# Kernel optimization log

Hardware: AMD Instinct MI355X
Metric: run time of the kernel (lower is better)

## Reference

```python
import jax, jax.numpy as jnp
import numpy as np

N_HEAD = 16
D_MODEL = 1024
D_HEAD = D_MODEL // N_HEAD  # 64
B, S = 1, 4096


def setup_inputs() -> dict:
    key = jax.random.key(0)
    ks = jax.random.split(key, 7)
    q = jax.random.normal(ks[0], (B, S, D_MODEL), dtype=jnp.float32)
    k = jax.random.normal(ks[1], (B, S, D_MODEL), dtype=jnp.float32)
    v = jax.random.normal(ks[2], (B, S, D_MODEL), dtype=jnp.float32)
    mask = jnp.ones((S, S), dtype=bool)
    # params match torch.rand init (uniform [0,1)); use uniform here too
    w_q = jax.random.uniform(ks[3], (D_MODEL, D_MODEL), dtype=jnp.float32)
    w_k = jax.random.uniform(ks[4], (D_HEAD, D_MODEL), dtype=jnp.float32)
    w_v = jax.random.uniform(ks[5], (D_HEAD, D_MODEL), dtype=jnp.float32)
    w_out = jax.random.uniform(ks[6], (D_MODEL, D_MODEL), dtype=jnp.float32)
    return {"q": q, "k": k, "v": v, "mask": mask,
            "w_q": w_q, "w_k": w_k, "w_v": w_v, "w_out": w_out}


def reference(q, k, v, mask, w_q, w_k, w_v, w_out):
    # F.linear(x, W) == x @ W.T
    query = q @ w_q.T                      # [b, n, d_model]
    key = k @ w_k.T                        # [b, s, d_head]  (single shared KV head)
    value = v @ w_v.T                      # [b, s, d_head]
    b, n, _ = query.shape
    query = query.reshape(b, n, N_HEAD, D_HEAD).transpose(0, 2, 1, 3)  # b h n d
    scores = jnp.einsum('bhnd,bsd->bhns', query, key) / jnp.sqrt(jnp.float32(D_HEAD))
    scores = jnp.where(mask[None, None], scores, jnp.float32(-jnp.inf))
    attn = jax.nn.softmax(scores, axis=-1)             # [b, h, n, s]
    out = jnp.einsum('bhns,bsd->bhnd', attn, value)    # [b, h, n, d]
    out = out.transpose(0, 2, 1, 3).reshape(b, n, D_MODEL)
    return out @ w_out.T
```

## Files before the change

### kernel.cpp

```cpp
#include <hip/hip_runtime.h>
#include <cstdint>
#include <cstddef>

#define S_LEN   4096
#define DM      1024
#define NHEAD   16
#define DH      64

typedef short bf16x8 __attribute__((ext_vector_type(8)));
typedef _Float16 f16x8 __attribute__((ext_vector_type(8)));
typedef float f32x4  __attribute__((ext_vector_type(4)));

__device__ __forceinline__ unsigned short f2bf(float x) {
    uint32_t u = __float_as_uint(x);
    u += 0x7fffu + ((u >> 16) & 1u);
    return (unsigned short)(u >> 16);
}
__device__ __forceinline__ float bf2f(unsigned short u) {
    return __uint_as_float(((uint32_t)u) << 16);
}
__device__ __forceinline__ unsigned pack_bf2(float a, float b) {
    return (unsigned)f2bf(a) | ((unsigned)f2bf(b) << 16);
}
__device__ __forceinline__ unsigned short f2h(float x) {
    _Float16 h = (_Float16)x;
    return __builtin_bit_cast(unsigned short, h);
}
__device__ __forceinline__ unsigned pack_h2(float a, float b) {
    return __builtin_bit_cast(unsigned, __builtin_amdgcn_cvt_pkrtz(a, b));
}
__device__ __forceinline__ void gl_lds16(const unsigned short* g, unsigned short* l) {
    __builtin_amdgcn_global_load_lds(
        (const __attribute__((address_space(1))) unsigned int*)g,
        (__attribute__((address_space(3))) unsigned int*)l, 16, 0, 0);
}
__device__ __forceinline__ void split8(const float4& a0, const float4& a1,
                                       ushort4& h0, ushort4& h1,
                                       ushort4& l0, ushort4& l1) {
    h0.x = f2bf(a0.x); l0.x = f2bf(a0.x - bf2f(h0.x));
    h0.y = f2bf(a0.y); l0.y = f2bf(a0.y - bf2f(h0.y));
    h0.z = f2bf(a0.z); l0.z = f2bf(a0.z - bf2f(h0.z));
    h0.w = f2bf(a0.w); l0.w = f2bf(a0.w - bf2f(h0.w));
    h1.x = f2bf(a1.x); l1.x = f2bf(a1.x - bf2f(h1.x));
    h1.y = f2bf(a1.y); l1.y = f2bf(a1.y - bf2f(h1.y));
    h1.z = f2bf(a1.z); l1.z = f2bf(a1.z - bf2f(h1.z));
    h1.w = f2bf(a1.w); l1.w = f2bf(a1.w - bf2f(h1.w));
}

__global__ void cvt_qw(const float* __restrict__ q, const float* __restrict__ wq,
                       const float* __restrict__ wo,
                       unsigned short* __restrict__ qh, unsigned short* __restrict__ ql,
                       unsigned short* __restrict__ wqh, unsigned short* __restrict__ wql,
                       unsigned short* __restrict__ woh)
{
    const int G1 = 1048576, GW = 262144;
    int i = blockIdx.x * blockDim.x + threadIdx.x;
    const float* src; unsigned short* h; unsigned short* l = nullptr; int off;
    if (i < G1)            { src = q;  h = qh;  l = ql;  off = i; }
    else if (i < G1 + GW)  { src = wq; h = wqh; l = wql; off = i - G1; }
    else                   { src = wo; h = woh;          off = i - G1 - GW; }
    float4 vv = reinterpret_cast<const float4*>(src)[off];
    ushort4 hh;
    hh.x = f2bf(vv.x); hh.y = f2bf(vv.y); hh.z = f2bf(vv.z); hh.w = f2bf(vv.w);
    reinterpret_cast<ushort4*>(h)[off] = hh;
    if (l) {
        ushort4 ll;
        ll.x = f2bf(vv.x - bf2f(hh.x)); ll.y = f2bf(vv.y - bf2f(hh.y));
        ll.z = f2bf(vv.z - bf2f(hh.z)); ll.w = f2bf(vv.w - bf2f(hh.w));
        reinterpret_cast<ushort4*>(l)[off] = ll;
    }
}

__launch_bounds__(256)
__global__ void kv_proj(const float* __restrict__ kin, const float* __restrict__ vin,
                        const float* __restrict__ wk, const float* __restrict__ wv,
                        unsigned short* __restrict__ Kf, unsigned short* __restrict__ Vtf)
{
    __shared__ unsigned short As_h[64][72];
    __shared__ unsigned short Bs_h[64][72];
    __shared__ unsigned short As_l[64][72];
    __shared__ unsigned short Bs_l[64][72];

    const int tid  = threadIdx.x;
    const int wave = tid >> 6;
    const int lane = tid & 63;
    const int lm   = lane & 15;
    const int quad = lane >> 4;
    const int m0   = blockIdx.x * 64;
    const bool isK = (blockIdx.y == 0);
    const float* A = isK ? kin : vin;
    const float* B = isK ? wk : wv;

    f32x4 acc[4] = {};

    for (int kc = 0; kc < DM; kc += 64) {
        __syncthreads();
#pragma unroll
        for (int i = 0; i < 2; ++i) {
            int c   = tid + i * 256;
            int r   = c >> 3;
            int col = (c & 7) * 8;
            float4 a0 = *(const float4*)&A[(size_t)(m0 + r) * DM + kc + col];
            float4 a1 = *(const float4*)&A[(size_t)(m0 + r) * DM + kc + col + 4];
            float4 b0 = *(const float4*)&B[(size_t)r * DM + kc + col];
            float4 b1 = *(const float4*)&B[(size_t)r * DM + kc + col + 4];
            ushort4 h0, h1, l0, l1;
            split8(a0, a1, h0, h1, l0, l1);
            *(ushort4*)&As_h[r][col] = h0;  *(ushort4*)&As_h[r][col + 4] = h1;
            if (isK) { *(ushort4*)&As_l[r][col] = l0;  *(ushort4*)&As_l[r][col + 4] = l1; }
            split8(b0, b1, h0, h1, l0, l1);
            *(ushort4*)&Bs_h[r][col] = h0;  *(ushort4*)&Bs_h[r][col + 4] = h1;
            if (isK) { *(ushort4*)&Bs_l[r][col] = l0;  *(ushort4*)&Bs_l[r][col + 4] = l1; }
        }
        __syncthreads();
#pragma unroll
        for (int kk = 0; kk < 64; kk += 32) {
            bf16x8 bh = *(const bf16x8*)&Bs_h[wave * 16 + lm][kk + quad * 8];
            bf16x8 bl;
            if (isK) bl = *(const bf16x8*)&Bs_l[wave * 16 + lm][kk + quad * 8];
#pragma unroll
            for (int ms = 0; ms < 4; ++ms) {
                bf16x8 ah = *(const bf16x8*)&As_h[ms * 16 + lm][kk + quad * 8];
                acc[ms] = __builtin_amdgcn_mfma_f32_16x16x32_bf16(ah, bh, acc[ms], 0, 0, 0);
                if (isK) {
                    bf16x8 al = *(const bf16x8*)&As_l[ms * 16 + lm][kk + quad * 8];
                    acc[ms] = __builtin_amdgcn_mfma_f32_16x16x32_bf16(ah, bl, acc[ms], 0, 0, 0);
                    acc[ms] = __builtin_amdgcn_mfma_f32_16x16x32_bf16(al, bh, acc[ms], 0, 0, 0);
                }
            }
        }
    }

#pragma unroll
    for (int ms = 0; ms < 4; ++ms)
#pragma unroll
        for (int r = 0; r < 4; ++r) {
            int row = m0 + ms * 16 + quad * 4 + r;
            int col = wave * 16 + lm;
            if (isK) Kf[(size_t)row * DH + col] = f2h(acc[ms][r]);
            else     Vtf[(size_t)col * S_LEN + row] = f2h(acc[ms][r]);
        }
}

__launch_bounds__(256)
__global__ void gemm_big(const unsigned short* __restrict__ Ah,
                         const unsigned short* __restrict__ Al,
                         const unsigned short* __restrict__ Bh,
                         const unsigned short* __restrict__ Bl,
                         unsigned short* __restrict__ Ch,
                         int M, int N, int K, int ldc)
{
    __shared__ unsigned short As_h[2][8192];
    __shared__ unsigned short Bs_h[2][8192];
    __shared__ unsigned short As_l[2][8192];
    __shared__ unsigned short Bs_l[2][8192];

    const int tid  = threadIdx.x;
    const int wave = tid >> 6;
    const int lane = tid & 63;
    const int lm   = lane & 15;
    const int quad = lane >> 4;
    const int wm   = wave >> 1;
    const int wn   = wave & 1;
    const int m0   = blockIdx.x * 128;
    const int n0   = blockIdx.y * 128;

    int srow[4], scol[4];
#pragma unroll
    for (int i = 0; i < 4; ++i) {
        int f = i * 256 + tid;
        srow[i] = f >> 3;
        scol[i] = ((f & 7) ^ (srow[i] & 7)) * 8;
    }

    auto stage = [&](int b, int kc) {
#pragma unroll
        for (int i = 0; i < 4; ++i) {
            const int dst = (i * 256 + wave * 64) * 8;
            gl_lds16(&Ah[(size_t)(m0 + srow[i]) * K + kc + scol[i]], &As_h[b][dst]);
            gl_lds16(&Bh[(size_t)(n0 + srow[i]) * K + kc + scol[i]], &Bs_h[b][dst]);
            gl_lds16(&Al[(size_t)(m0 + srow[i]) * K + kc + scol[i]], &As_l[b][dst]);
            gl_lds16(&Bl[(size_t)(n0 + srow[i]) * K + kc + scol[i]], &Bs_l[b][dst]);
        }
    };

    stage(0, 0);

    f32x4 acc[4][4] = {};
    const int nkc = K / 64;

    for (int it = 0; it < nkc; ++it) {
        const int b = it & 1;
        __syncthreads();
        if (it + 1 < nkc) stage(b ^ 1, (it + 1) * 64);

#pragma unroll
        for (int kk = 0; kk < 2; ++kk) {
            bf16x8 bh[4], bl[4];
#pragma unroll
            for (int ns = 0; ns < 4; ++ns) {
                const int off = (wn * 64 + ns * 16 + lm) * 64 + ((kk * 4 + quad) ^ (lm & 7)) * 8;
                bh[ns] = *(const bf16x8*)&Bs_h[b][off];
                bl[ns] = *(const bf16x8*)&Bs_l[b][off];
            }
#pragma unroll
            for (int ms = 0; ms < 4; ++ms) {
                const int off = (wm * 64 + ms * 16 + lm) * 64 + ((kk * 4 + quad) ^ (lm & 7)) * 8;
                bf16x8 ah = *(const bf16x8*)&As_h[b][off];
                bf16x8 al = *(const bf16x8*)&As_l[b][off];
#pragma unroll
                for (int ns = 0; ns < 4; ++ns) {
                    acc[ms][ns] = __builtin_amdgcn_mfma_f32_16x16x32_bf16(ah, bh[ns], acc[ms][ns], 0, 0, 0);
                    acc[ms][ns] = __builtin_amdgcn_mfma_f32_16x16x32_bf16(ah, bl[ns], acc[ms][ns], 0, 0, 0);
                    acc[ms][ns] = __builtin_amdgcn_mfma_f32_16x16x32_bf16(al, bh[ns], acc[ms][ns], 0, 0, 0);
                }
            }
        }
    }

#pragma unroll
    for (int ms = 0; ms < 4; ++ms)
#pragma unroll
        for (int ns = 0; ns < 4; ++ns)
#pragma unroll
            for (int r = 0; r < 4; ++r) {
                int row = m0 + wm * 64 + ms * 16 + quad * 4 + r;
                int col = n0 + wn * 64 + ns * 16 + lm;
                Ch[(size_t)row * ldc + col] = f2h(acc[ms][ns][r]);
            }
}

__launch_bounds__(256)
__global__ void flash_kernel(const unsigned short* __restrict__ Qf,
                             const unsigned short* __restrict__ Kf,
                             const unsigned short* __restrict__ Vt,
                             unsigned short* __restrict__ Op,
                             float* __restrict__ Mb,
                             float* __restrict__ Lb)
{
    __shared__ unsigned short Ks[2][4096];
    __shared__ unsigned short Vs[2][4096];

    const int tid  = threadIdx.x;
    const int wave = tid >> 6;
    const int lane = tid & 63;
    const int lm   = lane & 15;
    const int quad = lane >> 4;
    const int q0   = blockIdx.x * 128;
    const int h    = blockIdx.y;
    const int sp   = blockIdx.z;
    const int kbase = sp * (S_LEN / 2);
    const float c  = 0.125f * 1.44269504f;

    const int r0 = tid >> 3,         c0 = ((tid & 7) ^ (r0 & 7)) * 8;
    const int r1 = (tid + 256) >> 3, c1 = ((tid & 7) ^ (r1 & 7)) * 8;
    const int ldsA = wave * 512;
    const int ldsB = 2048 + wave * 512;

    auto stage = [&](int kt, int b) {
        gl_lds16(&Kf[(size_t)(kt + r0) * DH + c0], &Ks[b][ldsA]);
        gl_lds16(&Kf[(size_t)(kt + r1) * DH + c1], &Ks[b][ldsB]);
        gl_lds16(&Vt[(size_t)r0 * S_LEN + kt + c0], &Vs[b][ldsA]);
        gl_lds16(&Vt[(size_t)r1 * S_LEN + kt + c1], &Vs[b][ldsB]);
    };

    stage(kbase, 0);

    f16x8 qf[2][2];
#pragma unroll
    for (int nb = 0; nb < 2; ++nb)
#pragma unroll
        for (int kk = 0; kk < 2; ++kk) {
            size_t idx = (size_t)(q0 + wave * 32 + nb * 16 + lm) * DM + h * DH + kk * 32 + quad * 8;
            qf[nb][kk] = *(const f16x8*)&Qf[idx];
        }

    f32x4 oacc[2][4] = {};
    float m_run[2] = {-1e30f, -1e30f}, l_run[2] = {0.f, 0.f};

    for (int it = 0; it < 32; ++it) {
        const int b = it & 1;
        const int kt = kbase + it * 64;
        __syncthreads();
        if (it + 1 < 32) stage(kt + 64, b ^ 1);

        f32x4 sacc[2][4] = {};
#pragma unroll
        for (int kk = 0; kk < 2; ++kk) {
#pragma unroll
            for (int ms = 0; ms < 4; ++ms) {
                const int off = (ms * 16 + lm) * 64 + ((4 * kk + quad) ^ (lm & 7)) * 8;
                f16x8 kfr = *(const f16x8*)&Ks[b][off];
#pragma unroll
                for (int nb = 0; nb < 2; ++nb)
                    sacc[nb][ms] = __builtin_amdgcn_mfma_f32_16x16x32_f16(kfr, qf[nb][kk], sacc[nb][ms], 0, 0, 0);
            }
        }

        float mn[2];
#pragma unroll
        for (int nb = 0; nb < 2; ++nb) {
            float mx = -1e30f;
#pragma unroll
            for (int ms = 0; ms < 4; ++ms)
#pragma unroll
                for (int r = 0; r < 4; ++r) mx = fmaxf(mx, sacc[nb][ms][r]);
            mx = fmaxf(mx, __shfl_xor(mx, 16));
            mx = fmaxf(mx, __shfl_xor(mx, 32));
            mn[nb] = fmaxf(m_run[nb], mx);
        }

        if (__any((mn[0] > m_run[0]) || (mn[1] > m_run[1]))) {
#pragma unroll
            for (int mq = 0; mq < 2; ++mq) {
                float alpha = __builtin_amdgcn_exp2f((m_run[mq] - mn[mq]) * c);
                l_run[mq] *= alpha;
                m_run[mq] = mn[mq];
                float ar[4];
#pragma unroll
                for (int r = 0; r < 4; ++r) ar[r] = __shfl(alpha, quad * 4 + r);
#pragma unroll
                for (int nd = 0; nd < 4; ++nd)
#pragma unroll
                    for (int r = 0; r < 4; ++r) oacc[mq][nd][r] *= ar[r];
            }
        }

        unsigned pk[2][4][2];
#pragma unroll
        for (int nb = 0; nb < 2; ++nb) {
            float mc = m_run[nb] * c;
            float ps = 0.f;
#pragma unroll
            for (int ms = 0; ms < 4; ++ms) {
                float pr[4];
#pragma unroll
                for (int r = 0; r < 4; ++r) {
                    pr[r] = __builtin_amdgcn_exp2f(fmaf(sacc[nb][ms][r], c, -mc));
                    ps += pr[r];
                }
                pk[nb][ms][0] = pack_h2(pr[0], pr[1]);
                pk[nb][ms][1] = pack_h2(pr[2], pr[3]);
            }
            ps += __shfl_xor(ps, 16);
            ps += __shfl_xor(ps, 32);
            l_run[nb] += ps;
        }

#pragma unroll
        for (int kb = 0; kb < 2; ++kb) {
            f16x8 pa[2];
#pragma unroll
            for (int nb = 0; nb < 2; ++nb) {
                unsigned af[4] __attribute__((aligned(16)));
#pragma unroll
                for (int d = 0; d < 4; ++d) {
                    int srcl = ((2 * quad + (d >> 1)) & 3) * 16 + lm;
                    unsigned v_lo = (unsigned)__shfl((int)pk[nb][2 * kb][d & 1], srcl);
                    unsigned v_hi = (unsigned)__shfl((int)pk[nb][2 * kb + 1][d & 1], srcl);
                    af[d] = (quad < 2) ? v_lo : v_hi;
                }
                pa[nb] = *(f16x8*)af;
            }
#pragma unroll
            for (int nd = 0; nd < 4; ++nd) {
                const int off = (nd * 16 + lm) * 64 + ((4 * kb + quad) ^ (lm & 7)) * 8;
                f16x8 vb = *(const f16x8*)&Vs[b][off];
#pragma unroll
                for (int nb = 0; nb < 2; ++nb)
                    oacc[nb][nd] = __builtin_amdgcn_mfma_f32_16x16x32_f16(pa[nb], vb, oacc[nb][nd], 0, 0, 0);
            }
        }
    }

    unsigned short* Osp = Op + (size_t)sp * NHEAD * S_LEN * DH;
#pragma unroll
    for (int mq = 0; mq < 2; ++mq) {
#pragma unroll
        for (int nd = 0; nd < 4; ++nd)
#pragma unroll
            for (int r = 0; r < 4; ++r) {
                int q = q0 + wave * 32 + mq * 16 + quad * 4 + r;
                Osp[((size_t)h * S_LEN + q) * DH + nd * 16 + lm] = f2bf(oacc[mq][nd][r]);
            }
        if (quad == 0) {
            int q = q0 + wave * 32 + mq * 16 + lm;
            Mb[(size_t)sp * NHEAD * S_LEN + h * S_LEN + q] = m_run[mq];
            Lb[(size_t)sp * NHEAD * S_LEN + h * S_LEN + q] = l_run[mq];
        }
    }
}

__launch_bounds__(256)
__global__ void out_proj(const unsigned short* __restrict__ Op,
                         const float* __restrict__ Mb,
                         const float* __restrict__ Lb,
                         const unsigned short* __restrict__ Wo,
                         float* __restrict__ out)
{
    __shared__ unsigned short As[64][72];
    __shared__ unsigned short Bs[64][72];

    const int tid  = threadIdx.x;
    const int wave = tid >> 6;
    const int lane = tid & 63;
    const int lm   = lane & 15;
    const int quad = lane >> 4;
    const int m0   = blockIdx.x * 64;
    const int n0   = blockIdx.y * 64;
    const float c  = 0.125f * 1.44269504f;
    const int HS   = NHEAD * S_LEN;
    const size_t OSP = (size_t)NHEAD * S_LEN * DH;

    f32x4 acc[4] = {};

    for (int it = 0; it < 16; ++it) {
        __syncthreads();
#pragma unroll
        for (int i = 0; i < 2; ++i) {
            int cc  = tid + i * 256;
            int r   = cc >> 3;
            int col = (cc & 7) * 8;
            int q   = m0 + r;
            int hq  = it * S_LEN + q;
            float m1 = Mb[hq], m2 = Mb[HS + hq];
            float l1 = Lb[hq], l2 = Lb[HS + hq];
            float mm = fmaxf(m1, m2);
            float w1 = __builtin_amdgcn_exp2f((m1 - mm) * c);
            float w2 = __builtin_amdgcn_exp2f((m2 - mm) * c);
            float inv = 1.0f / (l1 * w1 + l2 * w2);
            w1 *= inv; w2 *= inv;
            size_t base = ((size_t)it * S_LEN + q) * DH + col;
            uint4 u1 = *(const uint4*)&Op[base];
            uint4 u2 = *(const uint4*)&Op[OSP + base];
            unsigned mrg[4];
            const unsigned* p1 = (const unsigned*)&u1;
            const unsigned* p2 = (const unsigned*)&u2;
#pragma unroll
            for (int d = 0; d < 4; ++d) {
                float a = bf2f((unsigned short)(p1[d] & 0xffff)) * w1
                        + bf2f((unsigned short)(p2[d] & 0xffff)) * w2;
                float b = bf2f((unsigned short)(p1[d] >> 16)) * w1
                        + bf2f((unsigned short)(p2[d] >> 16)) * w2;
                mrg[d] = pack_bf2(a, b);
            }
            *(uint4*)&As[r][col] = *(uint4*)mrg;
            *(uint4*)&Bs[r][col] = *(const uint4*)&Wo[(size_t)(n0 + r) * DM + it * 64 + col];
        }
        __syncthreads();
#pragma unroll
        for (int kk = 0; kk < 64; kk += 32) {
            bf16x8 bh = *(const bf16x8*)&Bs[wave * 16 + lm][kk + quad * 8];
#pragma unroll
            for (int ms = 0; ms < 4; ++ms) {
                bf16x8 ah = *(const bf16x8*)&As[ms * 16 + lm][kk + quad * 8];
                acc[ms] = __builtin_amdgcn_mfma_f32_16x16x32_bf16(ah, bh, acc[ms], 0, 0, 0);
            }
        }
    }

#pragma unroll
    for (int ms = 0; ms < 4; ++ms)
#pragma unroll
        for (int r = 0; r < 4; ++r) {
            int row = m0 + ms * 16 + quad * 4 + r;
            int col = n0 + wave * 16 + lm;
            out[(size_t)row * DM + col] = acc[ms][r];
        }
}

extern "C" void kernel_launch(void* const* d_in, const int* in_sizes, int n_in,
                              void* d_out, int out_size, void* d_ws, size_t ws_size,
                              hipStream_t stream)
{
    (void)in_sizes; (void)n_in; (void)out_size; (void)ws_size;
    const float* q     = (const float*)d_in[0];
    const float* k     = (const float*)d_in[1];
    const float* v     = (const float*)d_in[2];
    const float* w_q   = (const float*)d_in[4];
    const float* w_k   = (const float*)d_in[5];
    const float* w_v   = (const float*)d_in[6];
    const float* w_out = (const float*)d_in[7];
    float* out = (float*)d_out;

    char* ws = (char*)d_ws;
    size_t off = 0;
    auto alloc = [&](size_t bytes) -> unsigned short* {
        unsigned short* p = (unsigned short*)(ws + off);
        off += (bytes + 255) & ~(size_t)255;
        return p;
    };
    const size_t SZ_QKV = (size_t)S_LEN * DM * 2;
    const size_t SZ_WQ  = (size_t)DM * DM * 2;
    const size_t SZ_KV  = (size_t)S_LEN * DH * 2;

    unsigned short* qh  = alloc(SZ_QKV);
    unsigned short* ql  = alloc(SZ_QKV);
    unsigned short* wqh = alloc(SZ_WQ);
    unsigned short* wql = alloc(SZ_WQ);
    unsigned short* woh = alloc(SZ_WQ);
    unsigned short* Qf  = alloc(SZ_QKV);
    unsigned short* Kf  = alloc(SZ_KV);
    unsigned short* Vtf = alloc(SZ_KV);
    unsigned short* Op  = alloc(2 * NHEAD * SZ_KV);
    float* Mb = (float*)alloc(2 * NHEAD * S_LEN * 4);
    float* Lb = (float*)alloc(2 * NHEAD * S_LEN * 4);

    kv_proj<<<dim3(64, 2), 256, 0, stream>>>(k, v, w_k, w_v, Kf, Vtf);

    cvt_qw<<<dim3(6144), 256, 0, stream>>>(q, w_q, w_out, qh, ql, wqh, wql, woh);

    gemm_big<<<dim3(32, 8), 256, 0, stream>>>(qh, ql, wqh, wql, Qf, S_LEN, DM, DM, DM);

    flash_kernel<<<dim3(32, 16, 2), 256, 0, stream>>>(Qf, Kf, Vtf, Op, Mb, Lb);

    out_proj<<<dim3(64, 16), 256, 0, stream>>>(Op, Mb, Lb, woh, out);
}
```

Measured before the change: 376.8 us.

## Drop flash split-K, normalize in-kernel, reuse tiled GEMM for output projection

Merges the KV projection and the conversion kernels into one launch. The flash kernel no longer splits the key range: each 128-thread block handles 64 queries over all keys, normalizes by the softmax denominator in-kernel, and writes bf16 output directly in [n, d_model] layout. The separate merge and output-projection kernel is replaced by a single-term instantiation of the double-buffered 128x128 GEMM that writes fp32. This removes the partial-output and max/sum buffers and the merge pass, but each flash block now walks twice as many keys with fewer waves per block.

```diff
diff --git a/kernel.cpp b/kernel.cpp
--- a/kernel.cpp
+++ b/kernel.cpp
@@ -18,9 +18,6 @@
 }
 __device__ __forceinline__ float bf2f(unsigned short u) {
     return __uint_as_float(((uint32_t)u) << 16);
-}
-__device__ __forceinline__ unsigned pack_bf2(float a, float b) {
-    return (unsigned)f2bf(a) | ((unsigned)f2bf(b) << 16);
 }
 __device__ __forceinline__ unsigned short f2h(float x) {
     _Float16 h = (_Float16)x;
@@ -47,47 +44,50 @@
     h1.w = f2bf(a1.w); l1.w = f2bf(a1.w - bf2f(h1.w));
 }
 
-__global__ void cvt_qw(const float* __restrict__ q, const float* __restrict__ wq,
-                       const float* __restrict__ wo,
-                       unsigned short* __restrict__ qh, unsigned short* __restrict__ ql,
-                       unsigned short* __restrict__ wqh, unsigned short* __restrict__ wql,
-                       unsigned short* __restrict__ woh)
-{
-    const int G1 = 1048576, GW = 262144;
-    int i = blockIdx.x * blockDim.x + threadIdx.x;
-    const float* src; unsigned short* h; unsigned short* l = nullptr; int off;
-    if (i < G1)            { src = q;  h = qh;  l = ql;  off = i; }
-    else if (i < G1 + GW)  { src = wq; h = wqh; l = wql; off = i - G1; }
-    else                   { src = wo; h = woh;          off = i - G1 - GW; }
-    float4 vv = reinterpret_cast<const float4*>(src)[off];
-    ushort4 hh;
-    hh.x = f2bf(vv.x); hh.y = f2bf(vv.y); hh.z = f2bf(vv.z); hh.w = f2bf(vv.w);
-    reinterpret_cast<ushort4*>(h)[off] = hh;
-    if (l) {
-        ushort4 ll;
-        ll.x = f2bf(vv.x - bf2f(hh.x)); ll.y = f2bf(vv.y - bf2f(hh.y));
-        ll.z = f2bf(vv.z - bf2f(hh.z)); ll.w = f2bf(vv.w - bf2f(hh.w));
-        reinterpret_cast<ushort4*>(l)[off] = ll;
-    }
-}
-
 __launch_bounds__(256)
-__global__ void kv_proj(const float* __restrict__ kin, const float* __restrict__ vin,
-                        const float* __restrict__ wk, const float* __restrict__ wv,
-                        unsigned short* __restrict__ Kf, unsigned short* __restrict__ Vtf)
+__global__ void pre_kernel(const float* __restrict__ kin, const float* __restrict__ vin,
+                           const float* __restrict__ wk, const float* __restrict__ wv,
+                           const float* __restrict__ q, const float* __restrict__ wq,
+                           const float* __restrict__ wo,
+                           unsigned short* __restrict__ Kf, unsigned short* __restrict__ Vtf,
+                           unsigned short* __restrict__ qh, unsigned short* __restrict__ ql,
+                           unsigned short* __restrict__ wqh, unsigned short* __restrict__ wql,
+                           unsigned short* __restrict__ woh)
 {
     __shared__ unsigned short As_h[64][72];
     __shared__ unsigned short Bs_h[64][72];
     __shared__ unsigned short As_l[64][72];
     __shared__ unsigned short Bs_l[64][72];
 
-    const int tid  = threadIdx.x;
+    const int tid = threadIdx.x;
+    const int bx  = blockIdx.x;
+
+    if (bx >= 128) {
+        const int G1 = 1048576, GW = 262144;
+        int i = (bx - 128) * 256 + tid;
+        const float* src; unsigned short* h; unsigned short* l = nullptr; int off;
+        if (i < G1)            { src = q;  h = qh;  l = ql;  off = i; }
+        else if (i < G1 + GW)  { src = wq; h = wqh; l = wql; off = i - G1; }
+        else                   { src = wo; h = woh;          off = i - G1 - GW; }
+        float4 vv = reinterpret_cast<const float4*>(src)[off];
+        ushort4 hh;
+        hh.x = f2bf(vv.x); hh.y = f2bf(vv.y); hh.z = f2bf(vv.z); hh.w = f2bf(vv.w);
+        reinterpret_cast<ushort4*>(h)[off] = hh;
+        if (l) {
+            ushort4 ll;
+            ll.x = f2bf(vv.x - bf2f(hh.x)); ll.y = f2bf(vv.y - bf2f(hh.y));
+            ll.z = f2bf(vv.z - bf2f(hh.z)); ll.w = f2bf(vv.w - bf2f(hh.w));
+            reinterpret_cast<ushort4*>(l)[off] = ll;
+        }
+        return;
+    }
+
     const int wave = tid >> 6;
     const int lane = tid & 63;
     const int lm   = lane & 15;
     const int quad = lane >> 4;
-    const int m0   = blockIdx.x * 64;
-    const bool isK = (blockIdx.y == 0);
+    const bool isK = (bx < 64);
+    const int m0   = (bx & 63) * 64;
     const float* A = isK ? kin : vin;
     const float* B = isK ? wk : wv;
 
@@ -142,18 +142,20 @@
         }
 }
 
+template<int TERMS, int MODE>
 __launch_bounds__(256)
 __global__ void gemm_big(const unsigned short* __restrict__ Ah,
                          const unsigned short* __restrict__ Al,
                          const unsigned short* __restrict__ Bh,
                          const unsigned short* __restrict__ Bl,
                          unsigned short* __restrict__ Ch,
+                         float* __restrict__ Cf,
                          int M, int N, int K, int ldc)
 {
     __shared__ unsigned short As_h[2][8192];
     __shared__ unsigned short Bs_h[2][8192];
-    __shared__ unsigned short As_l[2][8192];
-    __shared__ unsigned short Bs_l[2][8192];
+    __shared__ unsigned short As_l[TERMS == 3 ? 2 : 1][TERMS == 3 ? 8192 : 1];
+    __shared__ unsigned short Bs_l[TERMS == 3 ? 2 : 1][TERMS == 3 ? 8192 : 1];
 
     const int tid  = threadIdx.x;
     const int wave = tid >> 6;
@@ -179,8 +181,10 @@
             const int dst = (i * 256 + wave * 64) * 8;
             gl_lds16(&Ah[(size_t)(m0 + srow[i]) * K + kc + scol[i]], &As_h[b][dst]);
             gl_lds16(&Bh[(size_t)(n0 + srow[i]) * K + kc + scol[i]], &Bs_h[b][dst]);
-            gl_lds16(&Al[(size_t)(m0 + srow[i]) * K + kc + scol[i]], &As_l[b][dst]);
-            gl_lds16(&Bl[(size_t)(n0 + srow[i]) * K + kc + scol[i]], &Bs_l[b][dst]);
+            if (TERMS == 3) {
+                gl_lds16(&Al[(size_t)(m0 + srow[i]) * K + kc + scol[i]], &As_l[b][dst]);
+                gl_lds16(&Bl[(size_t)(n0 + srow[i]) * K + kc + scol[i]], &Bs_l[b][dst]);
+            }
         }
     };
 
@@ -201,18 +205,21 @@
             for (int ns = 0; ns < 4; ++ns) {
                 const int off = (wn * 64 + ns * 16 + lm) * 64 + ((kk * 4 + quad) ^ (lm & 7)) * 8;
                 bh[ns] = *(const bf16x8*)&Bs_h[b][off];
-                bl[ns] = *(const bf16x8*)&Bs_l[b][off];
+                if (TERMS == 3) bl[ns] = *(const bf16x8*)&Bs_l[b][off];
             }
 #pragma unroll
             for (int ms = 0; ms < 4; ++ms) {
                 const int off = (wm * 64 + ms * 16 + lm) * 64 + ((kk * 4 + quad) ^ (lm & 7)) * 8;
                 bf16x8 ah = *(const bf16x8*)&As_h[b][off];
-                bf16x8 al = *(const bf16x8*)&As_l[b][off];
+                bf16x8 al;
+                if (TERMS == 3) al = *(const bf16x8*)&As_l[b][off];
 #pragma unroll
                 for (int ns = 0; ns < 4; ++ns) {
                     acc[ms][ns] = __builtin_amdgcn_mfma_f32_16x16x32_bf16(ah, bh[ns], acc[ms][ns], 0, 0, 0);
-                    acc[ms][ns] = __builtin_amdgcn_mfma_f32_16x16x32_bf16(ah, bl[ns], acc[ms][ns], 0, 0, 0);
-                    acc[ms][ns] = __builtin_amdgcn_mfma_f32_16x16x32_bf16(al, bh[ns], acc[ms][ns], 0, 0, 0);
+                    if (TERMS == 3) {
+                        acc[ms][ns] = __builtin_amdgcn_mfma_f32_16x16x32_bf16(ah, bl[ns], acc[ms][ns], 0, 0, 0);
+                        acc[ms][ns] = __builtin_amdgcn_mfma_f32_16x16x32_bf16(al, bh[ns], acc[ms][ns], 0, 0, 0);
+                    }
                 }
             }
         }
@@ -226,17 +233,16 @@
             for (int r = 0; r < 4; ++r) {
                 int row = m0 + wm * 64 + ms * 16 + quad * 4 + r;
                 int col = n0 + wn * 64 + ns * 16 + lm;
-                Ch[(size_t)row * ldc + col] = f2h(acc[ms][ns][r]);
-            }
-}
-
-__launch_bounds__(256)
+                if (MODE == 2) Cf[(size_t)row * ldc + col] = acc[ms][ns][r];
+                else           Ch[(size_t)row * ldc + col] = f2h(acc[ms][ns][r]);
+            }
+}
+
+__launch_bounds__(128)
 __global__ void flash_kernel(const unsigned short* __restrict__ Qf,
                              const unsigned short* __restrict__ Kf,
                              const unsigned short* __restrict__ Vt,
-                             unsigned short* __restrict__ Op,
-                             float* __restrict__ Mb,
-                             float* __restrict__ Lb)
+                             unsigned short* __restrict__ O)
 {
     __shared__ unsigned short Ks[2][4096];
     __shared__ unsigned short Vs[2][4096];
@@ -246,25 +252,28 @@
     const int lane = tid & 63;
     const int lm   = lane & 15;
     const int quad = lane >> 4;
-    const int q0   = blockIdx.x * 128;
+    const int q0   = blockIdx.x * 64;
     const int h    = blockIdx.y;
-    const int sp   = blockIdx.z;
-    const int kbase = sp * (S_LEN / 2);
     const float c  = 0.125f * 1.44269504f;
 
-    const int r0 = tid >> 3,         c0 = ((tid & 7) ^ (r0 & 7)) * 8;
-    const int r1 = (tid + 256) >> 3, c1 = ((tid & 7) ^ (r1 & 7)) * 8;
-    const int ldsA = wave * 512;
-    const int ldsB = 2048 + wave * 512;
+    int srow[4], scol[4];
+#pragma unroll
+    for (int i = 0; i < 4; ++i) {
+        int f = i * 128 + tid;
+        srow[i] = f >> 3;
+        scol[i] = ((f & 7) ^ (srow[i] & 7)) * 8;
+    }
 
     auto stage = [&](int kt, int b) {
-        gl_lds16(&Kf[(size_t)(kt + r0) * DH + c0], &Ks[b][ldsA]);
-        gl_lds16(&Kf[(size_t)(kt + r1) * DH + c1], &Ks[b][ldsB]);
-        gl_lds16(&Vt[(size_t)r0 * S_LEN + kt + c0], &Vs[b][ldsA]);
-        gl_lds16(&Vt[(size_t)r1 * S_LEN + kt + c1], &Vs[b][ldsB]);
+#pragma unroll
+        for (int i = 0; i < 4; ++i) {
+            const int dst = i * 1024 + wave * 512;
+            gl_lds16(&Kf[(size_t)(kt + srow[i]) * DH + scol[i]], &Ks[b][dst]);
+            gl_lds16(&Vt[(size_t)srow[i] * S_LEN + kt + scol[i]], &Vs[b][dst]);
+        }
     };
 
-    stage(kbase, 0);
+    stage(0, 0);
 
     f16x8 qf[2][2];
 #pragma unroll
@@ -278,11 +287,11 @@
     f32x4 oacc[2][4] = {};
     float m_run[2] = {-1e30f, -1e30f}, l_run[2] = {0.f, 0.f};
 
-    for (int it = 0; it < 32; ++it) {
+    for (int it = 0; it < 64; ++it) {
         const int b = it & 1;
-        const int kt = kbase + it * 64;
+        const int kt = it * 64;
         __syncthreads();
-        if (it + 1 < 32) stage(kt + 64, b ^ 1);
+        if (it + 1 < 64) stage(kt + 64, b ^ 1);
 
         f32x4 sacc[2][4] = {};
 #pragma unroll
@@ -373,100 +382,19 @@
         }
     }
 
-    unsigned short* Osp = Op + (size_t)sp * NHEAD * S_LEN * DH;
 #pragma unroll
     for (int mq = 0; mq < 2; ++mq) {
+        float lr[4];
+#pragma unroll
+        for (int r = 0; r < 4; ++r) lr[r] = 1.0f / __shfl(l_run[mq], quad * 4 + r);
 #pragma unroll
         for (int nd = 0; nd < 4; ++nd)
 #pragma unroll
             for (int r = 0; r < 4; ++r) {
-                int q = q0 + wave * 32 + mq * 16 + quad * 4 + r;
-                Osp[((size_t)h * S_LEN + q) * DH + nd * 16 + lm] = f2bf(oacc[mq][nd][r]);
-            }
-        if (quad == 0) {
-            int q = q0 + wave * 32 + mq * 16 + lm;
-            Mb[(size_t)sp * NHEAD * S_LEN + h * S_LEN + q] = m_run[mq];
-            Lb[(size_t)sp * NHEAD * S_LEN + h * S_LEN + q] = l_run[mq];
-        }
-    }
-}
-
-__launch_bounds__(256)
-__global__ void out_proj(const unsigned short* __restrict__ Op,
-                         const float* __restrict__ Mb,
-                         const float* __restrict__ Lb,
-                         const unsigned short* __restrict__ Wo,
-                         float* __restrict__ out)
-{
-    __shared__ unsigned short As[64][72];
-    __shared__ unsigned short Bs[64][72];
-
-    const int tid  = threadIdx.x;
-    const int wave = tid >> 6;
-    const int lane = tid & 63;
-    const int lm   = lane & 15;
-    const int quad = lane >> 4;
-    const int m0   = blockIdx.x * 64;
-    const int n0   = blockIdx.y * 64;
-    const float c  = 0.125f * 1.44269504f;
-    const int HS   = NHEAD * S_LEN;
-    const size_t OSP = (size_t)NHEAD * S_LEN * DH;
-
-    f32x4 acc[4] = {};
-
-    for (int it = 0; it < 16; ++it) {
-        __syncthreads();
-#pragma unroll
-        for (int i = 0; i < 2; ++i) {
-            int cc  = tid + i * 256;
-            int r   = cc >> 3;
-            int col = (cc & 7) * 8;
-            int q   = m0 + r;
-            int hq  = it * S_LEN + q;
-            float m1 = Mb[hq], m2 = Mb[HS + hq];
-            float l1 = Lb[hq], l2 = Lb[HS + hq];
-            float mm = fmaxf(m1, m2);
-            float w1 = __builtin_amdgcn_exp2f((m1 - mm) * c);
-            float w2 = __builtin_amdgcn_exp2f((m2 - mm) * c);
-            float inv = 1.0f / (l1 * w1 + l2 * w2);
-            w1 *= inv; w2 *= inv;
-            size_t base = ((size_t)it * S_LEN + q) * DH + col;
-            uint4 u1 = *(const uint4*)&Op[base];
-            uint4 u2 = *(const uint4*)&Op[OSP + base];
-            unsigned mrg[4];
-            const unsigned* p1 = (const unsigned*)&u1;
-            const unsigned* p2 = (const unsigned*)&u2;
-#pragma unroll
-            for (int d = 0; d < 4; ++d) {
-                float a = bf2f((unsigned short)(p1[d] & 0xffff)) * w1
-                        + bf2f((unsigned short)(p2[d] & 0xffff)) * w2;
-                float b = bf2f((unsigned short)(p1[d] >> 16)) * w1
-                        + bf2f((unsigned short)(p2[d] >> 16)) * w2;
-                mrg[d] = pack_bf2(a, b);
-            }
-            *(uint4*)&As[r][col] = *(uint4*)mrg;
-            *(uint4*)&Bs[r][col] = *(const uint4*)&Wo[(size_t)(n0 + r) * DM + it * 64 + col];
-        }
-        __syncthreads();
-#pragma unroll
-        for (int kk = 0; kk < 64; kk += 32) {
-            bf16x8 bh = *(const bf16x8*)&Bs[wave * 16 + lm][kk + quad * 8];
-#pragma unroll
-            for (int ms = 0; ms < 4; ++ms) {
-                bf16x8 ah = *(const bf16x8*)&As[ms * 16 + lm][kk + quad * 8];
-                acc[ms] = __builtin_amdgcn_mfma_f32_16x16x32_bf16(ah, bh, acc[ms], 0, 0, 0);
-            }
-        }
-    }
-
-#pragma unroll
-    for (int ms = 0; ms < 4; ++ms)
-#pragma unroll
-        for (int r = 0; r < 4; ++r) {
-            int row = m0 + ms * 16 + quad * 4 + r;
-            int col = n0 + wave * 16 + lm;
-            out[(size_t)row * DM + col] = acc[ms][r];
-        }
+                int qq = q0 + wave * 32 + mq * 16 + quad * 4 + r;
+                O[(size_t)qq * DM + h * DH + nd * 16 + lm] = f2bf(oacc[mq][nd][r] * lr[r]);
+            }
+    }
 }
 
 extern "C" void kernel_launch(void* const* d_in, const int* in_sizes, int n_in,
@@ -502,17 +430,16 @@
     unsigned short* Qf  = alloc(SZ_QKV);
     unsigned short* Kf  = alloc(SZ_KV);
     unsigned short* Vtf = alloc(SZ_KV);
-    unsigned short* Op  = alloc(2 * NHEAD * SZ_KV);
-    float* Mb = (float*)alloc(2 * NHEAD * S_LEN * 4);
-    float* Lb = (float*)alloc(2 * NHEAD * S_LEN * 4);
-
-    kv_proj<<<dim3(64, 2), 256, 0, stream>>>(k, v, w_k, w_v, Kf, Vtf);
-
-    cvt_qw<<<dim3(6144), 256, 0, stream>>>(q, w_q, w_out, qh, ql, wqh, wql, woh);
-
-    gemm_big<<<dim3(32, 8), 256, 0, stream>>>(qh, ql, wqh, wql, Qf, S_LEN, DM, DM, DM);
-
-    flash_kernel<<<dim3(32, 16, 2), 256, 0, stream>>>(Qf, Kf, Vtf, Op, Mb, Lb);
-
-    out_proj<<<dim3(64, 16), 256, 0, stream>>>(Op, Mb, Lb, woh, out);
-}
+    unsigned short* Obf = alloc(SZ_QKV);
+
+    pre_kernel<<<dim3(6272), 256, 0, stream>>>(k, v, w_k, w_v, q, w_q, w_out,
+                                               Kf, Vtf, qh, ql, wqh, wql, woh);
+
+    gemm_big<3, 3><<<dim3(32, 8), 256, 0, stream>>>(qh, ql, wqh, wql, Qf, nullptr,
+                                                    S_LEN, DM, DM, DM);
+
+    flash_kernel<<<dim3(64, 16), 128, 0, stream>>>(Qf, Kf, Vtf, Obf);
+
+    gemm_big<1, 2><<<dim3(32, 8), 256, 0, stream>>>(Obf, nullptr, woh, nullptr, nullptr, out,
+                                                    S_LEN, DM, DM, DM);
+}
```

Result: faster. 357.7 us (-5.1%).
